# Kernel optimization log

Hardware: AMD Instinct MI355X
Metric: run time of the kernel (lower is better)

Reference implementation:

```python
import jax, jax.numpy as jnp
import numpy as np

WS = (8, 8)  # window_size
NUM_HEADS = 6


def _relative_position_index(ws):
    ch, cw = np.arange(ws[0]), np.arange(ws[1])
    coords = np.stack(np.meshgrid(ch, cw, indexing='ij'))  # [2, Wh, Ww]
    cf = coords.reshape(2, -1)  # [2, N]
    rel = cf[:, :, None] - cf[:, None, :]  # [2, N, N]
    rel = rel.transpose(1, 2, 0).astype(np.int64)
    rel[:, :, 0] += ws[0] - 1
    rel[:, :, 1] += ws[1] - 1
    rel[:, :, 0] *= 2 * ws[1] - 1
    return rel.sum(-1)  # [N, N]

_RPI = jnp.asarray(_relative_position_index(WS))  # [64, 64] int


def setup_inputs() -> dict:
    key = jax.random.key(0)
    ks = jax.random.split(key, 6)
    B_, N, C = 4096, WS[0] * WS[1], 192
    return {
        'x': jax.random.normal(ks[0], (B_, N, C), jnp.float32),
        'qkv_w': jax.random.normal(ks[1], (3 * C, C), jnp.float32) * 0.02,
        'qkv_b': jax.random.normal(ks[2], (3 * C,), jnp.float32) * 0.02,
        'proj_w': jax.random.normal(ks[3], (C, C), jnp.float32) * 0.02,
        'proj_b': jax.random.normal(ks[4], (C,), jnp.float32) * 0.02,
        'rpb_table': jax.random.normal(ks[5], ((2 * WS[0] - 1) * (2 * WS[1] - 1), NUM_HEADS), jnp.float32) * 0.02,
    }


def reference(x, qkv_w, qkv_b, proj_w, proj_b, rpb_table):
    B_, N, C = x.shape
    H = NUM_HEADS
    D = C // H
    scale = D ** (-0.5)
    # qkv: torch Linear -> x @ W^T + b
    qkv = (x @ qkv_w.T + qkv_b).reshape(B_, N, 3, H, D)
    qkv = jnp.transpose(qkv, (2, 0, 3, 1, 4))  # [3, B_, H, N, D]
    q, k, v = qkv[0] * scale, qkv[1], qkv[2]
    attn = jnp.einsum('bhnd,bhmd->bhnm', q, k)  # [B_, H, N, N]
    bias = rpb_table[_RPI]  # [N, N, H]
    attn = attn + jnp.transpose(bias, (2, 0, 1))[None]  # broadcast over B_
    attn = jax.nn.softmax(attn, axis=-1)
    out = jnp.einsum('bhnm,bhmd->bnhd', attn, v).reshape(B_, N, C)
    return out @ proj_w.T + proj_b
```

## Files before the change

kernel.cpp:

```cpp
#include <hip/hip_runtime.h>
#include <hip/hip_bf16.h>

typedef short bf16x8 __attribute__((ext_vector_type(8)));
typedef float f32x4 __attribute__((ext_vector_type(4)));
typedef unsigned int u32;
typedef unsigned int u32x2 __attribute__((ext_vector_type(2)));

#define MFMA16 __builtin_amdgcn_mfma_f32_16x16x32_bf16
#define SCALE 0.17677669529663687f
#define LOG2E 1.4426950408889634f

#define OS_OFF 395520
#define WS_NEED (395520 + 100663296)

__device__ __forceinline__ unsigned short f2b(float x) {
  u32 u = __float_as_uint(x);
  u = (u + 0x7FFFu + ((u >> 16) & 1u)) >> 16;
  return (unsigned short)u;
}
__device__ __forceinline__ u32 pk2(float a, float b) {
  __hip_bfloat162 h = __float22bfloat162_rn(float2{a, b});
  return *(u32*)&h;
}
__device__ __forceinline__ uint2 pk4(f32x4 v) {
  return make_uint2(pk2(v[0], v[1]), pk2(v[2], v[3]));
}

__device__ __forceinline__ bf16x8 xpose(f32x4 a0, f32x4 a1) {
  u32 s0 = pk2(a0[0], a0[1]);
  u32 s1 = pk2(a0[2], a0[3]);
  u32 s2 = pk2(a1[0], a1[1]);
  u32 s3 = pk2(a1[2], a1[3]);
  u32x2 r0 = __builtin_amdgcn_permlane16_swap(s0, s2, false, false);
  u32x2 r1 = __builtin_amdgcn_permlane16_swap(s1, s3, false, false);
  union {
    u32 w[4];
    bf16x8 v;
  } u;
  u.w[0] = r0[0];
  u.w[1] = r1[0];
  u.w[2] = r0[1];
  u.w[3] = r1[1];
  return u.v;
}

__global__ void prep_kernel(const float* __restrict__ qkv_w, const float* __restrict__ qkv_b,
                            const float* __restrict__ proj_w, const float* __restrict__ rpb,
                            unsigned short* __restrict__ wqkv, unsigned short* __restrict__ wproj,
                            float* __restrict__ biasar, float* __restrict__ bq) {
  int i0 = blockIdx.x * blockDim.x + threadIdx.x;
  int stride = gridDim.x * blockDim.x;
  for (int i = i0; i < 576 * 192; i += stride) {
    float v = qkv_w[i];
    if (i < 192 * 192) v *= SCALE * LOG2E;
    wqkv[i] = f2b(v);
  }
  for (int i = i0; i < 192 * 192; i += stride) wproj[i] = f2b(proj_w[i]);
  for (int i = i0; i < 576; i += stride) {
    float v = qkv_b[i];
    if (i < 192) v *= SCALE * LOG2E;
    bq[i] = v;
  }
  for (int i = i0; i < 6 * 16 * 64 * 4; i += stride) {
    int r = i & 3;
    int lane = (i >> 2) & 63;
    int fid = (i >> 8) & 15;
    int h = i >> 12;
    int mt = fid >> 2, nt = fid & 3;
    int m = mt * 16 + (lane >> 4) * 4 + r;
    int n = nt * 16 + (lane & 15);
    int idx = ((n >> 3) - (m >> 3) + 7) * 15 + ((n & 7) - (m & 7) + 7);
    biasar[i] = rpb[idx * 6 + h] * LOG2E;
  }
}

__global__ void __launch_bounds__(256, 3) win_attn4(
    const float* __restrict__ x, const unsigned short* __restrict__ wqkv,
    const float* __restrict__ biasar, const float* __restrict__ bq,
    unsigned short* __restrict__ osout) {
  __shared__ __align__(16) char smem[25600];
  const int bid = blockIdx.x;
  const int xcd = bid & 7;
  const int local = bid >> 3;
  const int wl = local / 3;
  const int hg = local - wl * 3;
  const int b = xcd * 512 + wl;
  const int tid = threadIdx.x;
  const int wv = tid >> 6;
  const int hl = wv >> 1;
  const int head = hg * 2 + hl;
  const int half = wv & 1;
  const int lane = tid & 63;
  const int g = lane >> 4;
  const int c = lane & 15;
  char* xs = smem;
  char* exch = smem;

  float4 v[12];
  {
    const float* xb = x + (size_t)b * 12288;
#pragma unroll
    for (int it = 0; it < 12; ++it) {
      int idx = tid + it * 256;
      int tok = idx / 48, c4 = idx - tok * 48;
      v[it] = *(const float4*)(xb + tok * 192 + c4 * 4);
    }
  }

  bf16x8 wqf[2][6];
  {
    const unsigned short* wq0 = wqkv + (size_t)(head * 32 + c) * 192 + 8 * g;
    const unsigned short* wq1 = wq0 + 16 * 192;
#pragma unroll
    for (int kt = 0; kt < 6; ++kt) {
      wqf[0][kt] = *(const bf16x8*)(wq0 + kt * 32);
      wqf[1][kt] = *(const bf16x8*)(wq1 + kt * 32);
    }
  }

  {
#pragma unroll
    for (int it = 0; it < 12; ++it) {
      int idx = tid + it * 256;
      int tok = idx / 48, c4 = idx - tok * 48;
      *(uint2*)(xs + tok * 400 + c4 * 8) =
          make_uint2(pk2(v[it].x, v[it].y), pk2(v[it].z, v[it].w));
    }
  }
  __syncthreads();

  bf16x8 wkv[2][6];
  {
    const unsigned short* w0 =
        wqkv + (size_t)((half ? 384 : 192) + head * 32 + c) * 192 + 8 * g;
    const unsigned short* w1 = w0 + 16 * 192;
#pragma unroll
    for (int kt = 0; kt < 6; ++kt) {
      wkv[0][kt] = *(const bf16x8*)(w0 + kt * 32);
      wkv[1][kt] = *(const bf16x8*)(w1 + kt * 32);
    }
  }

  bf16x8 qb[2];
  {
    f32x4 a00 = *(const f32x4*)(bq + head * 32 + 4 * g);
    f32x4 a10 = *(const f32x4*)(bq + head * 32 + 16 + 4 * g);
    f32x4 a01 = a00, a11 = a10;
    const char* xr = xs + c * 400 + g * 16 + half * 12800;
#pragma unroll
    for (int kt = 0; kt < 6; ++kt) {
      bf16x8 x0 = *(const bf16x8*)(xr + kt * 64);
      bf16x8 x1 = *(const bf16x8*)(xr + 6400 + kt * 64);
      a00 = MFMA16(wqf[0][kt], x0, a00, 0, 0, 0);
      a10 = MFMA16(wqf[1][kt], x0, a10, 0, 0, 0);
      a01 = MFMA16(wqf[0][kt], x1, a01, 0, 0, 0);
      a11 = MFMA16(wqf[1][kt], x1, a11, 0, 0, 0);
    }
    qb[0] = xpose(a00, a10);
    qb[1] = xpose(a01, a11);
  }

  bf16x8 ka[4], va[2][2], own[4];
  {
    const char* xr = xs + c * 400 + g * 16;
    if (half == 0) {
      f32x4 bk0 = *(const f32x4*)(bq + 192 + head * 32 + 4 * g);
      f32x4 bk1 = *(const f32x4*)(bq + 192 + head * 32 + 16 + 4 * g);
      f32x4 ak[2][4];
#pragma unroll
      for (int tt = 0; tt < 4; ++tt) {
        ak[0][tt] = bk0;
        ak[1][tt] = bk1;
      }
#pragma unroll
      for (int kt = 0; kt < 6; ++kt) {
        bf16x8 xf0 = *(const bf16x8*)(xr + kt * 64);
        bf16x8 xf1 = *(const bf16x8*)(xr + 6400 + kt * 64);
        bf16x8 xf2 = *(const bf16x8*)(xr + 12800 + kt * 64);
        bf16x8 xf3 = *(const bf16x8*)(xr + 19200 + kt * 64);
        ak[0][0] = MFMA16(wkv[0][kt], xf0, ak[0][0], 0, 0, 0);
        ak[1][0] = MFMA16(wkv[1][kt], xf0, ak[1][0], 0, 0, 0);
        ak[0][1] = MFMA16(wkv[0][kt], xf1, ak[0][1], 0, 0, 0);
        ak[1][1] = MFMA16(wkv[1][kt], xf1, ak[1][1], 0, 0, 0);
        ak[0][2] = MFMA16(wkv[0][kt], xf2, ak[0][2], 0, 0, 0);
        ak[1][2] = MFMA16(wkv[1][kt], xf2, ak[1][2], 0, 0, 0);
        ak[0][3] = MFMA16(wkv[0][kt], xf3, ak[0][3], 0, 0, 0);
        ak[1][3] = MFMA16(wkv[1][kt], xf3, ak[1][3], 0, 0, 0);
      }
#pragma unroll
      for (int mt = 0; mt < 4; ++mt) own[mt] = ka[mt] = xpose(ak[0][mt], ak[1][mt]);
    } else {
      float bv0 = bq[384 + head * 32 + c];
      float bv1 = bq[384 + head * 32 + 16 + c];
      f32x4 av[4][2];
#pragma unroll
      for (int tt = 0; tt < 4; ++tt) {
        av[tt][0] = f32x4{bv0, bv0, bv0, bv0};
        av[tt][1] = f32x4{bv1, bv1, bv1, bv1};
      }
#pragma unroll
      for (int kt = 0; kt < 6; ++kt) {
        bf16x8 xf0 = *(const bf16x8*)(xr + kt * 64);
        bf16x8 xf1 = *(const bf16x8*)(xr + 6400 + kt * 64);
        bf16x8 xf2 = *(const bf16x8*)(xr + 12800 + kt * 64);
        bf16x8 xf3 = *(const bf16x8*)(xr + 19200 + kt * 64);
        av[0][0] = MFMA16(xf0, wkv[0][kt], av[0][0], 0, 0, 0);
        av[0][1] = MFMA16(xf0, wkv[1][kt], av[0][1], 0, 0, 0);
        av[1][0] = MFMA16(xf1, wkv[0][kt], av[1][0], 0, 0, 0);
        av[1][1] = MFMA16(xf1, wkv[1][kt], av[1][1], 0, 0, 0);
        av[2][0] = MFMA16(xf2, wkv[0][kt], av[2][0], 0, 0, 0);
        av[2][1] = MFMA16(xf2, wkv[1][kt], av[2][1], 0, 0, 0);
        av[3][0] = MFMA16(xf3, wkv[0][kt], av[3][0], 0, 0, 0);
        av[3][1] = MFMA16(xf3, wkv[1][kt], av[3][1], 0, 0, 0);
      }
#pragma unroll
      for (int dt = 0; dt < 2; ++dt)
#pragma unroll
        for (int kh = 0; kh < 2; ++kh)
          own[dt * 2 + kh] = va[dt][kh] = xpose(av[2 * kh][dt], av[2 * kh + 1][dt]);
    }
  }
  f32x4 bias[4][2];
  {
    const f32x4* bias4 = (const f32x4*)biasar + (size_t)(head * 16 + half * 2) * 64 + lane;
#pragma unroll
    for (int mt = 0; mt < 4; ++mt)
#pragma unroll
      for (int n2 = 0; n2 < 2; ++n2) bias[mt][n2] = bias4[(mt * 4 + n2) * 64];
  }
  __syncthreads();
  {
    char* ew = exch + hl * 8192 + half * 4096 + lane * 16;
#pragma unroll
    for (int f = 0; f < 4; ++f) *(bf16x8*)(ew + f * 1024) = own[f];
  }
  __syncthreads();
  {
    const char* er = exch + hl * 8192 + (half ^ 1) * 4096 + lane * 16;
    if (half == 0) {
#pragma unroll
      for (int f = 0; f < 4; ++f) va[f >> 1][f & 1] = *(const bf16x8*)(er + f * 1024);
    } else {
#pragma unroll
      for (int f = 0; f < 4; ++f) ka[f] = *(const bf16x8*)(er + f * 1024);
    }
  }

  bf16x8 pbf[2][2];
  float linv[2];
  {
    f32x4 s[4][2];
#pragma unroll
    for (int mt = 0; mt < 4; ++mt)
#pragma unroll
      for (int n2 = 0; n2 < 2; ++n2)
        s[mt][n2] = MFMA16(ka[mt], qb[n2], bias[mt][n2], 0, 0, 0);
#pragma unroll
    for (int n2 = 0; n2 < 2; ++n2) {
      float mx = fmaxf(fmaxf(fmaxf(s[0][n2][0], s[0][n2][1]), fmaxf(s[0][n2][2], s[0][n2][3])),
                       fmaxf(fmaxf(s[1][n2][0], s[1][n2][1]), fmaxf(s[1][n2][2], s[1][n2][3])));
      mx = fmaxf(mx, fmaxf(fmaxf(fmaxf(s[2][n2][0], s[2][n2][1]), fmaxf(s[2][n2][2], s[2][n2][3])),
                           fmaxf(fmaxf(s[3][n2][0], s[3][n2][1]), fmaxf(s[3][n2][2], s[3][n2][3]))));
      mx = fmaxf(mx, __shfl_xor(mx, 16));
      mx = fmaxf(mx, __shfl_xor(mx, 32));
      float sum = 0.0f;
#pragma unroll
      for (int mt = 0; mt < 4; ++mt)
#pragma unroll
        for (int r = 0; r < 4; ++r) {
          float e = __builtin_exp2f(s[mt][n2][r] - mx);
          s[mt][n2][r] = e;
          sum += e;
        }
      sum += __shfl_xor(sum, 16);
      sum += __shfl_xor(sum, 32);
      linv[n2] = 1.0f / sum;
    }
#pragma unroll
    for (int n2 = 0; n2 < 2; ++n2) {
      pbf[0][n2] = xpose(s[0][n2], s[1][n2]);
      pbf[1][n2] = xpose(s[2][n2], s[3][n2]);
    }
  }

  f32x4 o[2][2];
#pragma unroll
  for (int dt = 0; dt < 2; ++dt)
#pragma unroll
    for (int n2 = 0; n2 < 2; ++n2) o[dt][n2] = (f32x4)0.0f;
#pragma unroll
  for (int mh = 0; mh < 2; ++mh)
#pragma unroll
    for (int n2 = 0; n2 < 2; ++n2)
#pragma unroll
      for (int dt = 0; dt < 2; ++dt) o[dt][n2] = MFMA16(va[dt][mh], pbf[mh][n2], o[dt][n2], 0, 0, 0);

  uint2* dst = (uint2*)osout + ((size_t)((b * 6 + head) * 2 + half) * 4) * 64 + lane;
#pragma unroll
  for (int dt = 0; dt < 2; ++dt)
#pragma unroll
    for (int n2 = 0; n2 < 2; ++n2) {
#pragma unroll
      for (int r = 0; r < 4; ++r) o[dt][n2][r] *= linv[n2];
      dst[(dt * 2 + n2) * 64] = pk4(o[dt][n2]);
    }
}

__global__ void __launch_bounds__(256, 4) proj_kernel(
    const unsigned short* __restrict__ osin, const unsigned short* __restrict__ wproj,
    const float* __restrict__ proj_b, float* __restrict__ out) {
  __shared__ __align__(16) char smem[24576];
  const int b = blockIdx.x;
  const int tid = threadIdx.x;
  const int w = tid >> 6;
  const int lane = tid & 63;
  const int g = lane >> 4;
  const int c = lane & 15;

  {
    const uint2* src = (const uint2*)osin + (size_t)b * 3072;
#pragma unroll
    for (int it = 0; it < 12; ++it) {
      int i = tid + it * 256;
      int ls = i & 63;
      int f = (i >> 6) & 3;
      int unit = i >> 8;
      int head = unit >> 1, half = unit & 1;
      int dt = f >> 1, n2 = f & 1;
      int tok = half * 32 + n2 * 16 + (ls & 15);
      int d0 = head * 32 + dt * 16 + 4 * (ls >> 4);
      uint2 v = src[i];
      *(uint2*)(smem + tok * 384 + (((d0 >> 3) ^ (tok & 7)) << 4) + (d0 & 7) * 2) = v;
    }
  }
  __syncthreads();

  f32x4 acc[4][3];
#pragma unroll
  for (int mt = 0; mt < 4; ++mt)
#pragma unroll
    for (int ft = 0; ft < 3; ++ft) acc[mt][ft] = (f32x4)0.0f;
#pragma unroll
  for (int kt = 0; kt < 6; ++kt) {
    bf16x8 wf[3];
#pragma unroll
    for (int ft = 0; ft < 3; ++ft)
      wf[ft] = *(const bf16x8*)(wproj + (size_t)(w * 48 + ft * 16 + c) * 192 + kt * 32 + 8 * g);
#pragma unroll
    for (int mt = 0; mt < 4; ++mt) {
      bf16x8 of = *(const bf16x8*)(smem + (mt * 16 + c) * 384 + (((kt * 4 + g) ^ (c & 7)) << 4));
#pragma unroll
      for (int ft = 0; ft < 3; ++ft) acc[mt][ft] = MFMA16(of, wf[ft], acc[mt][ft], 0, 0, 0);
    }
  }
  float* outb = out + (size_t)b * 12288;
#pragma unroll
  for (int ft = 0; ft < 3; ++ft) {
    float pbv = proj_b[w * 48 + ft * 16 + c];
#pragma unroll
    for (int mt = 0; mt < 4; ++mt)
#pragma unroll
      for (int r = 0; r < 4; ++r)
        outb[(mt * 16 + 4 * g + r) * 192 + w * 48 + ft * 16 + c] = acc[mt][ft][r] + pbv;
  }
}

#define XFRAGOLD(tt, kt) \
  (*(const bf16x8*)(xs + ((tt) * 16 + c) * 384 + ((((kt) * 4 + g) ^ (c & 7)) << 4)))

__global__ void __launch_bounds__(384, 3) win_attn(
    const float* __restrict__ x, const unsigned short* __restrict__ wqkv,
    const unsigned short* __restrict__ wproj, const float* __restrict__ biasar,
    const float* __restrict__ bq, const float* __restrict__ proj_b, float* __restrict__ out) {
  __shared__ __align__(16) char smem[24576];
  const int b = blockIdx.x;
  const int tid = threadIdx.x;
  const int w = tid >> 6;
  const int lane = tid & 63;
  const int g = lane >> 4;
  const int c = lane & 15;
  char* xs = smem;

  {
    const float* xb = x + (size_t)b * 12288;
#pragma unroll
    for (int it = 0; it < 8; ++it) {
      int idx = tid + it * 384;
      int tok = idx / 48, c4 = idx % 48;
      float4 v = *(const float4*)(xb + tok * 192 + c4 * 4);
      *(uint2*)(xs + tok * 384 + (((c4 >> 1) ^ (tok & 7)) << 4) + (c4 & 1) * 8) =
          make_uint2(pk2(v.x, v.y), pk2(v.z, v.w));
    }
  }
  __syncthreads();

  bf16x8 qb[4];
  {
    f32x4 acc[2][4];
#pragma unroll
    for (int dt = 0; dt < 2; ++dt)
#pragma unroll
      for (int tt = 0; tt < 4; ++tt) acc[dt][tt] = (f32x4)0.0f;
#pragma unroll
    for (int kt = 0; kt < 6; ++kt) {
      bf16x8 wf[2];
#pragma unroll
      for (int dt = 0; dt < 2; ++dt)
        wf[dt] = *(const bf16x8*)(wqkv + (size_t)(w * 32 + dt * 16 + c) * 192 + kt * 32 + 8 * g);
#pragma unroll
      for (int tt = 0; tt < 4; ++tt) {
        bf16x8 xf = XFRAGOLD(tt, kt);
#pragma unroll
        for (int dt = 0; dt < 2; ++dt) acc[dt][tt] = MFMA16(wf[dt], xf, acc[dt][tt], 0, 0, 0);
      }
    }
#pragma unroll
    for (int dt = 0; dt < 2; ++dt)
#pragma unroll
      for (int r = 0; r < 4; ++r) {
        float bv = bq[w * 32 + dt * 16 + 4 * g + r];
#pragma unroll
        for (int tt = 0; tt < 4; ++tt) acc[dt][tt][r] += bv;
      }
#pragma unroll
    for (int nt = 0; nt < 4; ++nt) qb[nt] = xpose(acc[0][nt], acc[1][nt]);
  }

  bf16x8 ka[4];
  {
    f32x4 acc[2][4];
#pragma unroll
    for (int dt = 0; dt < 2; ++dt)
#pragma unroll
      for (int tt = 0; tt < 4; ++tt) acc[dt][tt] = (f32x4)0.0f;
#pragma unroll
    for (int kt = 0; kt < 6; ++kt) {
      bf16x8 wf[2];
#pragma unroll
      for (int dt = 0; dt < 2; ++dt)
        wf[dt] =
            *(const bf16x8*)(wqkv + (size_t)(192 + w * 32 + dt * 16 + c) * 192 + kt * 32 + 8 * g);
#pragma unroll
      for (int tt = 0; tt < 4; ++tt) {
        bf16x8 xf = XFRAGOLD(tt, kt);
#pragma unroll
        for (int dt = 0; dt < 2; ++dt) acc[dt][tt] = MFMA16(wf[dt], xf, acc[dt][tt], 0, 0, 0);
      }
    }
#pragma unroll
    for (int dt = 0; dt < 2; ++dt)
#pragma unroll
      for (int r = 0; r < 4; ++r) {
        float bv = bq[192 + w * 32 + dt * 16 + 4 * g + r];
#pragma unroll
        for (int tt = 0; tt < 4; ++tt) acc[dt][tt][r] += bv;
      }
#pragma unroll
    for (int mt = 0; mt < 4; ++mt) ka[mt] = xpose(acc[0][mt], acc[1][mt]);
  }

  bf16x8 pbf[2][4];
  float linv[4];
  const f32x4* bias4 = (const f32x4*)biasar;
#pragma unroll
  for (int h = 0; h < 2; ++h) {
    f32x4 s[4][2];
#pragma unroll
    for (int mt = 0; mt < 4; ++mt)
#pragma unroll
      for (int n2 = 0; n2 < 2; ++n2) {
        int nt = h * 2 + n2;
        f32x4 t = MFMA16(ka[mt], qb[nt], (f32x4)0.0f, 0, 0, 0);
        s[mt][n2] = t + bias4[(w * 16 + mt * 4 + nt) * 64 + lane];
      }
#pragma unroll
    for (int n2 = 0; n2 < 2; ++n2) {
      int nt = h * 2 + n2;
      float mx = -1e30f;
#pragma unroll
      for (int mt = 0; mt < 4; ++mt)
#pragma unroll
        for (int r = 0; r < 4; ++r) mx = fmaxf(mx, s[mt][n2][r]);
      mx = fmaxf(mx, __shfl_xor(mx, 16));
      mx = fmaxf(mx, __shfl_xor(mx, 32));
      float sum = 0.0f;
#pragma unroll
      for (int mt = 0; mt < 4; ++mt)
#pragma unroll
        for (int r = 0; r < 4; ++r) {
          float e = __builtin_exp2f(s[mt][n2][r] - mx);
          s[mt][n2][r] = e;
          sum += e;
        }
      sum += __shfl_xor(sum, 16);
      sum += __shfl_xor(sum, 32);
      linv[nt] = 1.0f / sum;
    }
#pragma unroll
    for (int n2 = 0; n2 < 2; ++n2) {
      pbf[0][h * 2 + n2] = xpose(s[0][n2], s[1][n2]);
      pbf[1][h * 2 + n2] = xpose(s[2][n2], s[3][n2]);
    }
  }

  bf16x8 va[2][2];
  {
    f32x4 acc[4][2];
#pragma unroll
    for (int mt = 0; mt < 4; ++mt)
#pragma unroll
      for (int dt = 0; dt < 2; ++dt) acc[mt][dt] = (f32x4)0.0f;
#pragma unroll
    for (int kt = 0; kt < 6; ++kt) {
      bf16x8 wf[2];
#pragma unroll
      for (int dt = 0; dt < 2; ++dt)
        wf[dt] =
            *(const bf16x8*)(wqkv + (size_t)(384 + w * 32 + dt * 16 + c) * 192 + kt * 32 + 8 * g);
#pragma unroll
      for (int tt = 0; tt < 4; ++tt) {
        bf16x8 xf = XFRAGOLD(tt, kt);
#pragma unroll
        for (int dt = 0; dt < 2; ++dt) acc[tt][dt] = MFMA16(xf, wf[dt], acc[tt][dt], 0, 0, 0);
      }
    }
#pragma unroll
    for (int dt = 0; dt < 2; ++dt) {
      float bv = bq[384 + w * 32 + dt * 16 + c];
#pragma unroll
      for (int mt = 0; mt < 4; ++mt)
#pragma unroll
        for (int r = 0; r < 4; ++r) acc[mt][dt][r] += bv;
    }
#pragma unroll
    for (int dt = 0; dt < 2; ++dt)
#pragma unroll
      for (int kh = 0; kh < 2; ++kh) va[dt][kh] = xpose(acc[2 * kh][dt], acc[2 * kh + 1][dt]);
  }

  f32x4 o[2][4];
#pragma unroll
  for (int dt = 0; dt < 2; ++dt)
#pragma unroll
    for (int nt = 0; nt < 4; ++nt) o[dt][nt] = (f32x4)0.0f;
#pragma unroll
  for (int mh = 0; mh < 2; ++mh)
#pragma unroll
    for (int nt = 0; nt < 4; ++nt)
#pragma unroll
      for (int dt = 0; dt < 2; ++dt) o[dt][nt] = MFMA16(va[dt][mh], pbf[mh][nt], o[dt][nt], 0, 0, 0);
#pragma unroll
  for (int dt = 0; dt < 2; ++dt)
#pragma unroll
    for (int nt = 0; nt < 4; ++nt)
#pragma unroll
      for (int r = 0; r < 4; ++r) o[dt][nt][r] *= linv[nt];

  __syncthreads();
#pragma unroll
  for (int dt = 0; dt < 2; ++dt)
#pragma unroll
    for (int nt = 0; nt < 4; ++nt)
      *(uint2*)(xs + (nt * 16 + c) * 384 + (((w * 4 + dt * 2 + (g >> 1)) ^ (c & 7)) << 4) +
                (g & 1) * 8) =
          make_uint2(pk2(o[dt][nt][0], o[dt][nt][1]), pk2(o[dt][nt][2], o[dt][nt][3]));
  __syncthreads();

  f32x4 accP[4][2];
#pragma unroll
  for (int mt = 0; mt < 4; ++mt)
#pragma unroll
    for (int ft = 0; ft < 2; ++ft) accP[mt][ft] = (f32x4)0.0f;
#pragma unroll
  for (int kt = 0; kt < 6; ++kt) {
    bf16x8 wp[2];
#pragma unroll
    for (int ft = 0; ft < 2; ++ft)
      wp[ft] = *(const bf16x8*)(wproj + (size_t)(w * 32 + ft * 16 + c) * 192 + kt * 32 + 8 * g);
#pragma unroll
    for (int mt = 0; mt < 4; ++mt) {
      bf16x8 of = *(const bf16x8*)(xs + (mt * 16 + c) * 384 + (((kt * 4 + g) ^ (c & 7)) << 4));
#pragma unroll
      for (int ft = 0; ft < 2; ++ft) accP[mt][ft] = MFMA16(of, wp[ft], accP[mt][ft], 0, 0, 0);
    }
  }
  float pb0 = proj_b[w * 32 + c];
  float pb1 = proj_b[w * 32 + 16 + c];
  float* outb = out + (size_t)b * 12288;
#pragma unroll
  for (int mt = 0; mt < 4; ++mt)
#pragma unroll
    for (int ft = 0; ft < 2; ++ft) {
      float pbv = ft ? pb1 : pb0;
#pragma unroll
      for (int r = 0; r < 4; ++r)
        outb[(mt * 16 + 4 * g + r) * 192 + w * 32 + ft * 16 + c] = accP[mt][ft][r] + pbv;
    }
}

extern "C" void kernel_launch(void* const* d_in, const int* in_sizes, int n_in,
                              void* d_out, int out_size, void* d_ws, size_t ws_size,
                              hipStream_t stream) {
  const float* x = (const float*)d_in[0];
  const float* qkv_w = (const float*)d_in[1];
  const float* qkv_b = (const float*)d_in[2];
  const float* proj_w = (const float*)d_in[3];
  const float* proj_b = (const float*)d_in[4];
  const float* rpb = (const float*)d_in[5];
  char* ws = (char*)d_ws;
  unsigned short* wqkv = (unsigned short*)ws;
  unsigned short* wproj = (unsigned short*)(ws + 221184);
  float* biasar = (float*)(ws + 294912);
  float* bqv = (float*)(ws + 393216);

  prep_kernel<<<432, 256, 0, stream>>>(qkv_w, qkv_b, proj_w, rpb, wqkv, wproj, biasar, bqv);

  if (ws_size >= (size_t)WS_NEED) {
    unsigned short* osbuf = (unsigned short*)(ws + OS_OFF);
    win_attn4<<<12288, 256, 0, stream>>>(x, wqkv, biasar, bqv, osbuf);
    proj_kernel<<<4096, 256, 0, stream>>>(osbuf, wproj, proj_b, (float*)d_out);
  } else {
    win_attn<<<4096, 384, 0, stream>>>(x, wqkv, wproj, biasar, bqv, proj_b, (float*)d_out);
  }
}
```

Before: 275.1 us.

## Process two windows per attention block, prefetching next window's input during compute

```diff
diff --git a/kernel.cpp b/kernel.cpp
--- a/kernel.cpp
+++ b/kernel.cpp
@@ -82,9 +82,9 @@
   const int bid = blockIdx.x;
   const int xcd = bid & 7;
   const int local = bid >> 3;
-  const int wl = local / 3;
-  const int hg = local - wl * 3;
-  const int b = xcd * 512 + wl;
+  const int u = local / 3;
+  const int hg = local - u * 3;
+  const int p = xcd * 256 + u;
   const int tid = threadIdx.x;
   const int wv = tid >> 6;
   const int hl = wv >> 1;
@@ -96,214 +96,224 @@
   char* xs = smem;
   char* exch = smem;
 
+  int stok[12], sc4[12];
+#pragma unroll
+  for (int it = 0; it < 12; ++it) {
+    int idx = tid + it * 256;
+    stok[it] = idx / 48;
+    sc4[it] = idx - stok[it] * 48;
+  }
+
   float4 v[12];
   {
-    const float* xb = x + (size_t)b * 12288;
-#pragma unroll
-    for (int it = 0; it < 12; ++it) {
-      int idx = tid + it * 256;
-      int tok = idx / 48, c4 = idx - tok * 48;
-      v[it] = *(const float4*)(xb + tok * 192 + c4 * 4);
-    }
-  }
-
-  bf16x8 wqf[2][6];
-  {
-    const unsigned short* wq0 = wqkv + (size_t)(head * 32 + c) * 192 + 8 * g;
-    const unsigned short* wq1 = wq0 + 16 * 192;
-#pragma unroll
-    for (int kt = 0; kt < 6; ++kt) {
-      wqf[0][kt] = *(const bf16x8*)(wq0 + kt * 32);
-      wqf[1][kt] = *(const bf16x8*)(wq1 + kt * 32);
-    }
-  }
-
-  {
-#pragma unroll
-    for (int it = 0; it < 12; ++it) {
-      int idx = tid + it * 256;
-      int tok = idx / 48, c4 = idx - tok * 48;
-      *(uint2*)(xs + tok * 400 + c4 * 8) =
+    const float* xb = x + (size_t)(2 * p) * 12288;
+#pragma unroll
+    for (int it = 0; it < 12; ++it) v[it] = *(const float4*)(xb + stok[it] * 192 + sc4[it] * 4);
+  }
+
+#pragma unroll
+  for (int wi = 0; wi < 2; ++wi) {
+    const int b = 2 * p + wi;
+
+#pragma unroll
+    for (int it = 0; it < 12; ++it)
+      *(uint2*)(xs + stok[it] * 400 + sc4[it] * 8) =
           make_uint2(pk2(v[it].x, v[it].y), pk2(v[it].z, v[it].w));
-    }
-  }
-  __syncthreads();
-
-  bf16x8 wkv[2][6];
-  {
-    const unsigned short* w0 =
-        wqkv + (size_t)((half ? 384 : 192) + head * 32 + c) * 192 + 8 * g;
-    const unsigned short* w1 = w0 + 16 * 192;
-#pragma unroll
-    for (int kt = 0; kt < 6; ++kt) {
-      wkv[0][kt] = *(const bf16x8*)(w0 + kt * 32);
-      wkv[1][kt] = *(const bf16x8*)(w1 + kt * 32);
-    }
-  }
-
-  bf16x8 qb[2];
-  {
-    f32x4 a00 = *(const f32x4*)(bq + head * 32 + 4 * g);
-    f32x4 a10 = *(const f32x4*)(bq + head * 32 + 16 + 4 * g);
-    f32x4 a01 = a00, a11 = a10;
-    const char* xr = xs + c * 400 + g * 16 + half * 12800;
-#pragma unroll
-    for (int kt = 0; kt < 6; ++kt) {
-      bf16x8 x0 = *(const bf16x8*)(xr + kt * 64);
-      bf16x8 x1 = *(const bf16x8*)(xr + 6400 + kt * 64);
-      a00 = MFMA16(wqf[0][kt], x0, a00, 0, 0, 0);
-      a10 = MFMA16(wqf[1][kt], x0, a10, 0, 0, 0);
-      a01 = MFMA16(wqf[0][kt], x1, a01, 0, 0, 0);
-      a11 = MFMA16(wqf[1][kt], x1, a11, 0, 0, 0);
-    }
-    qb[0] = xpose(a00, a10);
-    qb[1] = xpose(a01, a11);
-  }
-
-  bf16x8 ka[4], va[2][2], own[4];
-  {
-    const char* xr = xs + c * 400 + g * 16;
-    if (half == 0) {
-      f32x4 bk0 = *(const f32x4*)(bq + 192 + head * 32 + 4 * g);
-      f32x4 bk1 = *(const f32x4*)(bq + 192 + head * 32 + 16 + 4 * g);
-      f32x4 ak[2][4];
-#pragma unroll
-      for (int tt = 0; tt < 4; ++tt) {
-        ak[0][tt] = bk0;
-        ak[1][tt] = bk1;
-      }
+    __syncthreads();
+
+    if (wi == 0) {
+      const float* xb = x + (size_t)(2 * p + 1) * 12288;
+#pragma unroll
+      for (int it = 0; it < 12; ++it) v[it] = *(const float4*)(xb + stok[it] * 192 + sc4[it] * 4);
+    }
+
+    bf16x8 wqf[2][6];
+    {
+      const unsigned short* wq0 = wqkv + (size_t)(head * 32 + c) * 192 + 8 * g;
+      const unsigned short* wq1 = wq0 + 16 * 192;
 #pragma unroll
       for (int kt = 0; kt < 6; ++kt) {
-        bf16x8 xf0 = *(const bf16x8*)(xr + kt * 64);
-        bf16x8 xf1 = *(const bf16x8*)(xr + 6400 + kt * 64);
-        bf16x8 xf2 = *(const bf16x8*)(xr + 12800 + kt * 64);
-        bf16x8 xf3 = *(const bf16x8*)(xr + 19200 + kt * 64);
-        ak[0][0] = MFMA16(wkv[0][kt], xf0, ak[0][0], 0, 0, 0);
-        ak[1][0] = MFMA16(wkv[1][kt], xf0, ak[1][0], 0, 0, 0);
-        ak[0][1] = MFMA16(wkv[0][kt], xf1, ak[0][1], 0, 0, 0);
-        ak[1][1] = MFMA16(wkv[1][kt], xf1, ak[1][1], 0, 0, 0);
-        ak[0][2] = MFMA16(wkv[0][kt], xf2, ak[0][2], 0, 0, 0);
-        ak[1][2] = MFMA16(wkv[1][kt], xf2, ak[1][2], 0, 0, 0);
-        ak[0][3] = MFMA16(wkv[0][kt], xf3, ak[0][3], 0, 0, 0);
-        ak[1][3] = MFMA16(wkv[1][kt], xf3, ak[1][3], 0, 0, 0);
-      }
-#pragma unroll
-      for (int mt = 0; mt < 4; ++mt) own[mt] = ka[mt] = xpose(ak[0][mt], ak[1][mt]);
-    } else {
-      float bv0 = bq[384 + head * 32 + c];
-      float bv1 = bq[384 + head * 32 + 16 + c];
-      f32x4 av[4][2];
-#pragma unroll
-      for (int tt = 0; tt < 4; ++tt) {
-        av[tt][0] = f32x4{bv0, bv0, bv0, bv0};
-        av[tt][1] = f32x4{bv1, bv1, bv1, bv1};
-      }
+        wqf[0][kt] = *(const bf16x8*)(wq0 + kt * 32);
+        wqf[1][kt] = *(const bf16x8*)(wq1 + kt * 32);
+      }
+    }
+
+    bf16x8 qb[2];
+    {
+      f32x4 a00 = *(const f32x4*)(bq + head * 32 + 4 * g);
+      f32x4 a10 = *(const f32x4*)(bq + head * 32 + 16 + 4 * g);
+      f32x4 a01 = a00, a11 = a10;
+      const char* xr = xs + c * 400 + g * 16 + half * 12800;
 #pragma unroll
       for (int kt = 0; kt < 6; ++kt) {
-        bf16x8 xf0 = *(const bf16x8*)(xr + kt * 64);
-        bf16x8 xf1 = *(const bf16x8*)(xr + 6400 + kt * 64);
-        bf16x8 xf2 = *(const bf16x8*)(xr + 12800 + kt * 64);
-        bf16x8 xf3 = *(const bf16x8*)(xr + 19200 + kt * 64);
-        av[0][0] = MFMA16(xf0, wkv[0][kt], av[0][0], 0, 0, 0);
-        av[0][1] = MFMA16(xf0, wkv[1][kt], av[0][1], 0, 0, 0);
-        av[1][0] = MFMA16(xf1, wkv[0][kt], av[1][0], 0, 0, 0);
-        av[1][1] = MFMA16(xf1, wkv[1][kt], av[1][1], 0, 0, 0);
-        av[2][0] = MFMA16(xf2, wkv[0][kt], av[2][0], 0, 0, 0);
-        av[2][1] = MFMA16(xf2, wkv[1][kt], av[2][1], 0, 0, 0);
-        av[3][0] = MFMA16(xf3, wkv[0][kt], av[3][0], 0, 0, 0);
-        av[3][1] = MFMA16(xf3, wkv[1][kt], av[3][1], 0, 0, 0);
-      }
-#pragma unroll
-      for (int dt = 0; dt < 2; ++dt)
-#pragma unroll
-        for (int kh = 0; kh < 2; ++kh)
-          own[dt * 2 + kh] = va[dt][kh] = xpose(av[2 * kh][dt], av[2 * kh + 1][dt]);
-    }
-  }
-  f32x4 bias[4][2];
-  {
-    const f32x4* bias4 = (const f32x4*)biasar + (size_t)(head * 16 + half * 2) * 64 + lane;
-#pragma unroll
-    for (int mt = 0; mt < 4; ++mt)
-#pragma unroll
-      for (int n2 = 0; n2 < 2; ++n2) bias[mt][n2] = bias4[(mt * 4 + n2) * 64];
-  }
-  __syncthreads();
-  {
-    char* ew = exch + hl * 8192 + half * 4096 + lane * 16;
-#pragma unroll
-    for (int f = 0; f < 4; ++f) *(bf16x8*)(ew + f * 1024) = own[f];
-  }
-  __syncthreads();
-  {
-    const char* er = exch + hl * 8192 + (half ^ 1) * 4096 + lane * 16;
-    if (half == 0) {
-#pragma unroll
-      for (int f = 0; f < 4; ++f) va[f >> 1][f & 1] = *(const bf16x8*)(er + f * 1024);
-    } else {
-#pragma unroll
-      for (int f = 0; f < 4; ++f) ka[f] = *(const bf16x8*)(er + f * 1024);
-    }
-  }
-
-  bf16x8 pbf[2][2];
-  float linv[2];
-  {
-    f32x4 s[4][2];
-#pragma unroll
-    for (int mt = 0; mt < 4; ++mt)
+        bf16x8 x0 = *(const bf16x8*)(xr + kt * 64);
+        bf16x8 x1 = *(const bf16x8*)(xr + 6400 + kt * 64);
+        a00 = MFMA16(wqf[0][kt], x0, a00, 0, 0, 0);
+        a10 = MFMA16(wqf[1][kt], x0, a10, 0, 0, 0);
+        a01 = MFMA16(wqf[0][kt], x1, a01, 0, 0, 0);
+        a11 = MFMA16(wqf[1][kt], x1, a11, 0, 0, 0);
+      }
+      qb[0] = xpose(a00, a10);
+      qb[1] = xpose(a01, a11);
+    }
+
+    bf16x8 ka[4], va[2][2], own[4];
+    {
+      bf16x8 wkv[2][6];
+      const unsigned short* w0 =
+          wqkv + (size_t)((half ? 384 : 192) + head * 32 + c) * 192 + 8 * g;
+      const unsigned short* w1 = w0 + 16 * 192;
+#pragma unroll
+      for (int kt = 0; kt < 6; ++kt) {
+        wkv[0][kt] = *(const bf16x8*)(w0 + kt * 32);
+        wkv[1][kt] = *(const bf16x8*)(w1 + kt * 32);
+      }
+      const char* xr = xs + c * 400 + g * 16;
+      if (half == 0) {
+        f32x4 bk0 = *(const f32x4*)(bq + 192 + head * 32 + 4 * g);
+        f32x4 bk1 = *(const f32x4*)(bq + 192 + head * 32 + 16 + 4 * g);
+        f32x4 ak[2][4];
+#pragma unroll
+        for (int tt = 0; tt < 4; ++tt) {
+          ak[0][tt] = bk0;
+          ak[1][tt] = bk1;
+        }
+#pragma unroll
+        for (int kt = 0; kt < 6; ++kt) {
+          bf16x8 xf0 = *(const bf16x8*)(xr + kt * 64);
+          bf16x8 xf1 = *(const bf16x8*)(xr + 6400 + kt * 64);
+          bf16x8 xf2 = *(const bf16x8*)(xr + 12800 + kt * 64);
+          bf16x8 xf3 = *(const bf16x8*)(xr + 19200 + kt * 64);
+          ak[0][0] = MFMA16(wkv[0][kt], xf0, ak[0][0], 0, 0, 0);
+          ak[1][0] = MFMA16(wkv[1][kt], xf0, ak[1][0], 0, 0, 0);
+          ak[0][1] = MFMA16(wkv[0][kt], xf1, ak[0][1], 0, 0, 0);
+          ak[1][1] = MFMA16(wkv[1][kt], xf1, ak[1][1], 0, 0, 0);
+          ak[0][2] = MFMA16(wkv[0][kt], xf2, ak[0][2], 0, 0, 0);
+          ak[1][2] = MFMA16(wkv[1][kt], xf2, ak[1][2], 0, 0, 0);
+          ak[0][3] = MFMA16(wkv[0][kt], xf3, ak[0][3], 0, 0, 0);
+          ak[1][3] = MFMA16(wkv[1][kt], xf3, ak[1][3], 0, 0, 0);
+        }
+#pragma unroll
+        for (int mt = 0; mt < 4; ++mt) own[mt] = ka[mt] = xpose(ak[0][mt], ak[1][mt]);
+      } else {
+        float bv0 = bq[384 + head * 32 + c];
+        float bv1 = bq[384 + head * 32 + 16 + c];
+        f32x4 av[4][2];
+#pragma unroll
+        for (int tt = 0; tt < 4; ++tt) {
+          av[tt][0] = f32x4{bv0, bv0, bv0, bv0};
+          av[tt][1] = f32x4{bv1, bv1, bv1, bv1};
+        }
+#pragma unroll
+        for (int kt = 0; kt < 6; ++kt) {
+          bf16x8 xf0 = *(const bf16x8*)(xr + kt * 64);
+          bf16x8 xf1 = *(const bf16x8*)(xr + 6400 + kt * 64);
+          bf16x8 xf2 = *(const bf16x8*)(xr + 12800 + kt * 64);
+          bf16x8 xf3 = *(const bf16x8*)(xr + 19200 + kt * 64);
+          av[0][0] = MFMA16(xf0, wkv[0][kt], av[0][0], 0, 0, 0);
+          av[0][1] = MFMA16(xf0, wkv[1][kt], av[0][1], 0, 0, 0);
+          av[1][0] = MFMA16(xf1, wkv[0][kt], av[1][0], 0, 0, 0);
+          av[1][1] = MFMA16(xf1, wkv[1][kt], av[1][1], 0, 0, 0);
+          av[2][0] = MFMA16(xf2, wkv[0][kt], av[2][0], 0, 0, 0);
+          av[2][1] = MFMA16(xf2, wkv[1][kt], av[2][1], 0, 0, 0);
+          av[3][0] = MFMA16(xf3, wkv[0][kt], av[3][0], 0, 0, 0);
+          av[3][1] = MFMA16(xf3, wkv[1][kt], av[3][1], 0, 0, 0);
+        }
+#pragma unroll
+        for (int dt = 0; dt < 2; ++dt)
+#pragma unroll
+          for (int kh = 0; kh < 2; ++kh)
+            own[dt * 2 + kh] = va[dt][kh] = xpose(av[2 * kh][dt], av[2 * kh + 1][dt]);
+      }
+    }
+    f32x4 bias[4][2];
+    {
+      const f32x4* bias4 = (const f32x4*)biasar + (size_t)(head * 16 + half * 2) * 64 + lane;
+#pragma unroll
+      for (int mt = 0; mt < 4; ++mt)
+#pragma unroll
+        for (int n2 = 0; n2 < 2; ++n2) bias[mt][n2] = bias4[(mt * 4 + n2) * 64];
+    }
+    __syncthreads();
+    {
+      char* ew = exch + hl * 8192 + half * 4096 + lane * 16;
+#pragma unroll
+      for (int f = 0; f < 4; ++f) *(bf16x8*)(ew + f * 1024) = own[f];
+    }
+    __syncthreads();
+    {
+      const char* er = exch + hl * 8192 + (half ^ 1) * 4096 + lane * 16;
+      if (half == 0) {
+#pragma unroll
+        for (int f = 0; f < 4; ++f) va[f >> 1][f & 1] = *(const bf16x8*)(er + f * 1024);
+      } else {
+#pragma unroll
+        for (int f = 0; f < 4; ++f) ka[f] = *(const bf16x8*)(er + f * 1024);
+      }
+    }
+    if (wi == 0) __syncthreads();
+
+    bf16x8 pbf[2][2];
+    float linv[2];
+    {
+      f32x4 s[4][2];
+#pragma unroll
+      for (int mt = 0; mt < 4; ++mt)
+#pragma unroll
+        for (int n2 = 0; n2 < 2; ++n2)
+          s[mt][n2] = MFMA16(ka[mt], qb[n2], bias[mt][n2], 0, 0, 0);
+#pragma unroll
+      for (int n2 = 0; n2 < 2; ++n2) {
+        float mx = fmaxf(fmaxf(fmaxf(s[0][n2][0], s[0][n2][1]), fmaxf(s[0][n2][2], s[0][n2][3])),
+                         fmaxf(fmaxf(s[1][n2][0], s[1][n2][1]), fmaxf(s[1][n2][2], s[1][n2][3])));
+        mx = fmaxf(mx,
+                   fmaxf(fmaxf(fmaxf(s[2][n2][0], s[2][n2][1]), fmaxf(s[2][n2][2], s[2][n2][3])),
+                         fmaxf(fmaxf(s[3][n2][0], s[3][n2][1]), fmaxf(s[3][n2][2], s[3][n2][3]))));
+        mx = fmaxf(mx, __shfl_xor(mx, 16));
+        mx = fmaxf(mx, __shfl_xor(mx, 32));
+        float sum = 0.0f;
+#pragma unroll
+        for (int mt = 0; mt < 4; ++mt)
+#pragma unroll
+          for (int r = 0; r < 4; ++r) {
+            float e = __builtin_exp2f(s[mt][n2][r] - mx);
+            s[mt][n2][r] = e;
+            sum += e;
+          }
+        sum += __shfl_xor(sum, 16);
+        sum += __shfl_xor(sum, 32);
+        linv[n2] = 1.0f / sum;
+      }
+#pragma unroll
+      for (int n2 = 0; n2 < 2; ++n2) {
+        pbf[0][n2] = xpose(s[0][n2], s[1][n2]);
+        pbf[1][n2] = xpose(s[2][n2], s[3][n2]);
+      }
+    }
+
+    f32x4 o[2][2];
+#pragma unroll
+    for (int dt = 0; dt < 2; ++dt)
+#pragma unroll
+      for (int n2 = 0; n2 < 2; ++n2) o[dt][n2] = (f32x4)0.0f;
+#pragma unroll
+    for (int mh = 0; mh < 2; ++mh)
 #pragma unroll
       for (int n2 = 0; n2 < 2; ++n2)
-        s[mt][n2] = MFMA16(ka[mt], qb[n2], bias[mt][n2], 0, 0, 0);
-#pragma unroll
-    for (int n2 = 0; n2 < 2; ++n2) {
-      float mx = fmaxf(fmaxf(fmaxf(s[0][n2][0], s[0][n2][1]), fmaxf(s[0][n2][2], s[0][n2][3])),
-                       fmaxf(fmaxf(s[1][n2][0], s[1][n2][1]), fmaxf(s[1][n2][2], s[1][n2][3])));
-      mx = fmaxf(mx, fmaxf(fmaxf(fmaxf(s[2][n2][0], s[2][n2][1]), fmaxf(s[2][n2][2], s[2][n2][3])),
-                           fmaxf(fmaxf(s[3][n2][0], s[3][n2][1]), fmaxf(s[3][n2][2], s[3][n2][3]))));
-      mx = fmaxf(mx, __shfl_xor(mx, 16));
-      mx = fmaxf(mx, __shfl_xor(mx, 32));
-      float sum = 0.0f;
-#pragma unroll
-      for (int mt = 0; mt < 4; ++mt)
-#pragma unroll
-        for (int r = 0; r < 4; ++r) {
-          float e = __builtin_exp2f(s[mt][n2][r] - mx);
-          s[mt][n2][r] = e;
-          sum += e;
-        }
-      sum += __shfl_xor(sum, 16);
-      sum += __shfl_xor(sum, 32);
-      linv[n2] = 1.0f / sum;
-    }
-#pragma unroll
-    for (int n2 = 0; n2 < 2; ++n2) {
-      pbf[0][n2] = xpose(s[0][n2], s[1][n2]);
-      pbf[1][n2] = xpose(s[2][n2], s[3][n2]);
-    }
-  }
-
-  f32x4 o[2][2];
-#pragma unroll
-  for (int dt = 0; dt < 2; ++dt)
-#pragma unroll
-    for (int n2 = 0; n2 < 2; ++n2) o[dt][n2] = (f32x4)0.0f;
-#pragma unroll
-  for (int mh = 0; mh < 2; ++mh)
-#pragma unroll
-    for (int n2 = 0; n2 < 2; ++n2)
-#pragma unroll
-      for (int dt = 0; dt < 2; ++dt) o[dt][n2] = MFMA16(va[dt][mh], pbf[mh][n2], o[dt][n2], 0, 0, 0);
-
-  uint2* dst = (uint2*)osout + ((size_t)((b * 6 + head) * 2 + half) * 4) * 64 + lane;
-#pragma unroll
-  for (int dt = 0; dt < 2; ++dt)
-#pragma unroll
-    for (int n2 = 0; n2 < 2; ++n2) {
-#pragma unroll
-      for (int r = 0; r < 4; ++r) o[dt][n2][r] *= linv[n2];
-      dst[(dt * 2 + n2) * 64] = pk4(o[dt][n2]);
-    }
+#pragma unroll
+        for (int dt = 0; dt < 2; ++dt)
+          o[dt][n2] = MFMA16(va[dt][mh], pbf[mh][n2], o[dt][n2], 0, 0, 0);
+
+    uint2* dst = (uint2*)osout + ((size_t)((b * 6 + head) * 2 + half) * 4) * 64 + lane;
+#pragma unroll
+    for (int dt = 0; dt < 2; ++dt)
+#pragma unroll
+      for (int n2 = 0; n2 < 2; ++n2) {
+#pragma unroll
+        for (int r = 0; r < 4; ++r) o[dt][n2][r] *= linv[n2];
+        dst[(dt * 2 + n2) * 64] = pk4(o[dt][n2]);
+      }
+  }
 }
 
 __global__ void __launch_bounds__(256, 4) proj_kernel(
@@ -617,7 +627,7 @@
 
   if (ws_size >= (size_t)WS_NEED) {
     unsigned short* osbuf = (unsigned short*)(ws + OS_OFF);
-    win_attn4<<<12288, 256, 0, stream>>>(x, wqkv, biasar, bqv, osbuf);
+    win_attn4<<<6144, 256, 0, stream>>>(x, wqkv, biasar, bqv, osbuf);
     proj_kernel<<<4096, 256, 0, stream>>>(osbuf, wproj, proj_b, (float*)d_out);
   } else {
     win_attn<<<4096, 384, 0, stream>>>(x, wqkv, wproj, biasar, bqv, proj_b, (float*)d_out);
```

Result: slower. 371.3 us (+35.0%).
